# Kernel tuning notes

Hardware: AMD Instinct MI355X
Metric: run time of the kernel (lower is better)

Reference implementation:

```python
import jax, jax.numpy as jnp
import numpy as np

N, D_IN, D_HID, D_OUT, ORDER = 8192, 512, 1024, 64, 3

def setup_inputs() -> dict:
    key = jax.random.key(0)
    k = jax.random.split(key, 5)
    x = jax.random.normal(k[0], (N, D_IN), dtype=jnp.float32)
    adj = jax.random.uniform(k[1], (ORDER, N, N), dtype=jnp.float32)
    W1 = jax.random.normal(k[2], (ORDER, D_IN, D_HID), dtype=jnp.float32) * (1.0 / np.sqrt(D_IN))
    b1 = jnp.zeros((D_HID,), dtype=jnp.float32)
    W2 = jax.random.normal(k[3], (ORDER, D_HID, D_OUT), dtype=jnp.float32) * (1.0 / np.sqrt(D_HID))
    b2 = jnp.zeros((D_OUT,), dtype=jnp.float32)
    return {"x": x, "preprocessed": adj, "W1": W1, "b1": b1, "W2": W2, "b2": b2}

def multi_val_gc(x, adj, W, b):
    # x: [N, in], adj: [order, N, N], W: [order, in, out]
    xw = jnp.einsum('ni,kio->kno', x, W)          # [order, N, out]
    out = jnp.einsum('knm,kmo->no', adj, xw)      # sum over orders
    return out + b

def reference(x, preprocessed, W1, b1, W2, b2):
    h = multi_val_gc(x, preprocessed, W1, b1)
    h = jax.nn.relu(h)
    # dropout is identity in eval mode
    h = multi_val_gc(h, preprocessed, W2, b2)
    return jax.nn.log_softmax(h, axis=1)
```

## Files before the change

kernel.cpp:

```cpp
#include <hip/hip_runtime.h>
#include <hip/hip_bf16.h>
#include <cstdint>
#include <cstddef>


typedef __bf16 bf16_t;
typedef __bf16 bf16x8 __attribute__((ext_vector_type(8)));
typedef __bf16 bf16x4 __attribute__((ext_vector_type(4)));
typedef float  f32x4  __attribute__((ext_vector_type(4)));

#define NROWS 8192
#define DIN   512
#define DHID  1024
#define DOUT  64
#define ORD   3
#define KTOT  24576

#define GLDS(g, l) __builtin_amdgcn_global_load_lds( \
    (__attribute__((address_space(1))) void*)(g),    \
    (__attribute__((address_space(3))) void*)(l), 16, 0, 0)


__global__ void k_cvt_x(const float* __restrict__ x, bf16_t* __restrict__ xb) {
  int i = blockIdx.x * blockDim.x + threadIdx.x;
  const float4* p = reinterpret_cast<const float4*>(x) + (size_t)i * 2;
  float4 v0 = p[0], v1 = p[1];
  bf16x8 o;
  o[0]=(bf16_t)v0.x; o[1]=(bf16_t)v0.y; o[2]=(bf16_t)v0.z; o[3]=(bf16_t)v0.w;
  o[4]=(bf16_t)v1.x; o[5]=(bf16_t)v1.y; o[6]=(bf16_t)v1.z; o[7]=(bf16_t)v1.w;
  *reinterpret_cast<bf16x8*>(xb + (size_t)i * 8) = o;
}

__global__ void k_cvt_adj(const float* __restrict__ a, bf16_t* __restrict__ ab) {
  size_t i = (size_t)blockIdx.x * blockDim.x + threadIdx.x;
  const size_t stride = (size_t)gridDim.x * blockDim.x;
  const float4* src = reinterpret_cast<const float4*>(a);
#pragma unroll 4
  for (int it = 0; it < 48; ++it, i += stride) {
    float4 v0 = src[i * 2], v1 = src[i * 2 + 1];
    bf16x8 o;
    o[0]=(bf16_t)v0.x; o[1]=(bf16_t)v0.y; o[2]=(bf16_t)v0.z; o[3]=(bf16_t)v0.w;
    o[4]=(bf16_t)v1.x; o[5]=(bf16_t)v1.y; o[6]=(bf16_t)v1.z; o[7]=(bf16_t)v1.w;
    *reinterpret_cast<bf16x8*>(ab + i * 8) = o;
  }
}

__global__ void k_transpose_cvt(const float* __restrict__ src, bf16_t* __restrict__ dst,
                                int R, int C) {
  __shared__ float tile[64][65];
  int ord = blockIdx.z;
  src += (size_t)ord * R * C;
  dst += (size_t)ord * R * C;
  int c0 = blockIdx.x * 64, r0 = blockIdx.y * 64;
  for (int i = 0; i < 16; ++i) {
    int idx = i * 256 + threadIdx.x;
    int r = idx >> 6, c = idx & 63;
    tile[r][c] = src[(size_t)(r0 + r) * C + c0 + c];
  }
  __syncthreads();
  for (int i = 0; i < 16; ++i) {
    int idx = i * 256 + threadIdx.x;
    int cc = idx >> 6, rr = idx & 63;
    dst[(size_t)(c0 + cc) * R + r0 + rr] = (bf16_t)tile[rr][cc];
  }
}

__global__ __launch_bounds__(256) void k_gemm_xw1(
    const bf16_t* __restrict__ xb,
    const bf16_t* __restrict__ w1t,
    bf16_t* __restrict__ xw1t)
{
  __shared__ bf16_t As[128 * 64];
  __shared__ bf16_t Bs[128 * 64];
  int ntile = blockIdx.x, mtile = blockIdx.y, ord = blockIdx.z;
  int tid = threadIdx.x, lane = tid & 63, wid = tid >> 6;
  int wm = wid >> 1, wn = wid & 1;
  int sl = (lane & 7) ^ (lane >> 3);
  f32x4 acc[4][4] = {};
  const bf16_t* w1o = w1t + (size_t)ord * DHID * DIN;
  for (int kt = 0; kt < DIN; kt += 64) {
    for (int j = 0; j < 4; ++j) {
      int q = wid * 4 + j;
      int row = q * 8 + (lane >> 3);
      GLDS(xb + (size_t)(mtile * 128 + row) * DIN + kt + sl * 8, &As[q * 512]);
    }
    for (int j = 0; j < 4; ++j) {
      int q = wid * 4 + j;
      int row = q * 8 + (lane >> 3);
      GLDS(w1o + (size_t)(ntile * 128 + row) * DIN + kt + sl * 8, &Bs[q * 512]);
    }
    __syncthreads();
    for (int ks = 0; ks < 2; ++ks) {
      int psl = ((ks << 2) + (lane >> 4)) ^ (lane & 7);
      bf16x8 a[4], b[4];
      for (int f = 0; f < 4; ++f)
        a[f] = *reinterpret_cast<const bf16x8*>(&As[(wm * 64 + f * 16 + (lane & 15)) * 64 + psl * 8]);
      for (int f = 0; f < 4; ++f)
        b[f] = *reinterpret_cast<const bf16x8*>(&Bs[(wn * 64 + f * 16 + (lane & 15)) * 64 + psl * 8]);
      for (int fm = 0; fm < 4; ++fm)
        for (int fn = 0; fn < 4; ++fn)
          acc[fm][fn] = __builtin_amdgcn_mfma_f32_16x16x32_bf16(a[fm], b[fn], acc[fm][fn], 0, 0, 0);
    }
    __syncthreads();
  }
  for (int fm = 0; fm < 4; ++fm)
    for (int fn = 0; fn < 4; ++fn) {
      int o  = ntile * 128 + wn * 64 + fn * 16 + (lane & 15);
      int n0 = mtile * 128 + wm * 64 + fm * 16 + ((lane >> 4) << 2);
      bf16x4 v;
      v[0] = (bf16_t)acc[fm][fn][0]; v[1] = (bf16_t)acc[fm][fn][1];
      v[2] = (bf16_t)acc[fm][fn][2]; v[3] = (bf16_t)acc[fm][fn][3];
      *reinterpret_cast<bf16x4*>(&xw1t[(size_t)o * KTOT + ord * NROWS + n0]) = v;
    }
}

__global__ __launch_bounds__(512) void k_gemm_h256(
    const bf16_t* __restrict__ adjb,
    const bf16_t* __restrict__ xw1t,
    float* __restrict__ hpart)
{
  __shared__ bf16_t As[2][256 * 64];
  __shared__ bf16_t Bs[2][256 * 64];
  int d = blockIdx.x;
  int xcd = d & 7;
  int s = d >> 3;
  int ksp = xcd & 1;
  int mtile = (xcd >> 1) * 8 + (s >> 2);
  int ntile = s & 3;
  int tid = threadIdx.x, lane = tid & 63, wid = tid >> 6;
  int wm = wid >> 2, wn = wid & 3;
  int sl = (lane & 7) ^ (lane >> 3);
  const size_t NN = (size_t)NROWS * NROWS;
  f32x4 acc[8][4] = {};
  const int T0 = ksp * 192, NT = 192;

  auto stage = [&](int buf, int t) {
    int kk = (T0 + t) * 64;
    int ord = kk >> 13, mcol = kk & 8191;
    const bf16_t* ao = adjb + (size_t)ord * NN + (size_t)(mtile * 256) * NROWS + mcol;
#pragma unroll
    for (int j = 0; j < 4; ++j) {
      int q = wid * 4 + j;
      int row = q * 8 + (lane >> 3);
      GLDS(ao + (size_t)row * NROWS + sl * 8, &As[buf][q * 512]);
    }
#pragma unroll
    for (int j = 0; j < 4; ++j) {
      int q = wid * 4 + j;
      int row = q * 8 + (lane >> 3);
      GLDS(xw1t + (size_t)(ntile * 256 + row) * KTOT + kk + sl * 8, &Bs[buf][q * 512]);
    }
  };

  auto compute = [&](int cur) {
    const bf16_t* Ac = &As[cur][0];
    const bf16_t* Bc = &Bs[cur][0];
#pragma unroll
    for (int ks = 0; ks < 2; ++ks) {
      int psl = ((ks << 2) + (lane >> 4)) ^ (lane & 7);
      bf16x8 a[8], b[4];
#pragma unroll
      for (int f = 0; f < 8; ++f)
        a[f] = *reinterpret_cast<const bf16x8*>(&Ac[(wm * 128 + f * 16 + (lane & 15)) * 64 + psl * 8]);
#pragma unroll
      for (int f = 0; f < 4; ++f)
        b[f] = *reinterpret_cast<const bf16x8*>(&Bc[(wn * 64 + f * 16 + (lane & 15)) * 64 + psl * 8]);
#pragma unroll
      for (int fm = 0; fm < 8; ++fm)
#pragma unroll
        for (int fn = 0; fn < 4; ++fn)
          acc[fm][fn] = __builtin_amdgcn_mfma_f32_16x16x32_bf16(a[fm], b[fn], acc[fm][fn], 0, 0, 0);
    }
  };

  stage(0, 0);
  for (int t = 0; t < NT - 1; ++t) {
    int cur = t & 1;
    stage(cur ^ 1, t + 1);
    asm volatile("s_waitcnt vmcnt(8)" ::: "memory");
    __builtin_amdgcn_s_barrier();
    compute(cur);
    asm volatile("" ::: "memory");
    __builtin_amdgcn_s_barrier();
  }
  asm volatile("s_waitcnt vmcnt(0)" ::: "memory");
  __builtin_amdgcn_s_barrier();
  compute((NT - 1) & 1);

  float* pout = hpart + (size_t)ksp * NROWS * DHID;
#pragma unroll
  for (int fm = 0; fm < 8; ++fm)
#pragma unroll
    for (int fn = 0; fn < 4; ++fn) {
      int o  = ntile * 256 + wn * 64 + fn * 16 + (lane & 15);
      int n0 = mtile * 256 + wm * 128 + fm * 16 + ((lane >> 4) << 2);
      for (int j = 0; j < 4; ++j)
        pout[(size_t)(n0 + j) * DHID + o] = acc[fm][fn][j];
    }
}

__global__ void k_reduce_h(const float* __restrict__ hpart, const float* __restrict__ b1,
                           bf16_t* __restrict__ h) {
  size_t i4 = (size_t)blockIdx.x * blockDim.x + threadIdx.x;
  size_t base = i4 * 4;
  int col = (int)(base & (DHID - 1));
  const size_t S = (size_t)NROWS * DHID;
  float4 p0 = *reinterpret_cast<const float4*>(hpart + base);
  float4 p1 = *reinterpret_cast<const float4*>(hpart + S + base);
  float4 bb = *reinterpret_cast<const float4*>(b1 + col);
  bf16x4 v;
  float t0 = p0.x + p1.x + bb.x; v[0] = (bf16_t)(t0 > 0.f ? t0 : 0.f);
  float t1 = p0.y + p1.y + bb.y; v[1] = (bf16_t)(t1 > 0.f ? t1 : 0.f);
  float t2 = p0.z + p1.z + bb.z; v[2] = (bf16_t)(t2 > 0.f ? t2 : 0.f);
  float t3 = p0.w + p1.w + bb.w; v[3] = (bf16_t)(t3 > 0.f ? t3 : 0.f);
  *reinterpret_cast<bf16x4*>(h + base) = v;
}

__global__ __launch_bounds__(256) void k_gemm_h128(
    const bf16_t* __restrict__ adjb, const bf16_t* __restrict__ xw1t,
    const float* __restrict__ b1, bf16_t* __restrict__ h)
{
  __shared__ bf16_t As[2][128 * 64];
  __shared__ bf16_t Bs[2][128 * 64];
  int d = blockIdx.x;
  int xcd = d & 7;
  int idx = d >> 3;
  int mtile = xcd * 8 + (idx >> 3);
  int ntile = idx & 7;
  int tid = threadIdx.x, lane = tid & 63, wid = tid >> 6;
  int wm = wid >> 1, wn = wid & 1;
  int sl = (lane & 7) ^ (lane >> 3);
  const size_t NN = (size_t)NROWS * NROWS;
  f32x4 acc[4][4] = {};
  const int NT = KTOT / 64;

  auto stage = [&](int buf, int kt) {
    int kk = kt * 64;
    int ord = kk >> 13, mcol = kk & 8191;
    const bf16_t* ao = adjb + (size_t)ord * NN + (size_t)(mtile * 128) * NROWS + mcol;
#pragma unroll
    for (int jj = 0; jj < 4; ++jj) {
      int q = wid * 4 + jj;
      int row = q * 8 + (lane >> 3);
      GLDS(ao + (size_t)row * NROWS + sl * 8, &As[buf][q * 512]);
    }
#pragma unroll
    for (int jj = 0; jj < 4; ++jj) {
      int q = wid * 4 + jj;
      int row = q * 8 + (lane >> 3);
      GLDS(xw1t + (size_t)(ntile * 128 + row) * KTOT + kk + sl * 8, &Bs[buf][q * 512]);
    }
  };
  auto compute = [&](int cur) {
    const bf16_t* Ac = &As[cur][0];
    const bf16_t* Bc = &Bs[cur][0];
#pragma unroll
    for (int ks = 0; ks < 2; ++ks) {
      int psl = ((ks << 2) + (lane >> 4)) ^ (lane & 7);
      bf16x8 a[4], b[4];
      for (int f = 0; f < 4; ++f)
        a[f] = *reinterpret_cast<const bf16x8*>(&Ac[(wm * 64 + f * 16 + (lane & 15)) * 64 + psl * 8]);
      for (int f = 0; f < 4; ++f)
        b[f] = *reinterpret_cast<const bf16x8*>(&Bc[(wn * 64 + f * 16 + (lane & 15)) * 64 + psl * 8]);
      for (int fm = 0; fm < 4; ++fm)
        for (int fn = 0; fn < 4; ++fn)
          acc[fm][fn] = __builtin_amdgcn_mfma_f32_16x16x32_bf16(a[fm], b[fn], acc[fm][fn], 0, 0, 0);
    }
  };

  stage(0, 0);
  for (int t = 0; t < NT - 1; ++t) {
    int cur = t & 1;
    stage(cur ^ 1, t + 1);
    asm volatile("s_waitcnt vmcnt(8)" ::: "memory");
    __builtin_amdgcn_s_barrier();
    compute(cur);
    asm volatile("" ::: "memory");
    __builtin_amdgcn_s_barrier();
  }
  asm volatile("s_waitcnt vmcnt(0)" ::: "memory");
  __builtin_amdgcn_s_barrier();
  compute((NT - 1) & 1);

  for (int fm = 0; fm < 4; ++fm)
    for (int fn = 0; fn < 4; ++fn) {
      int o  = ntile * 128 + wn * 64 + fn * 16 + (lane & 15);
      float bias = b1[o];
      int n0 = mtile * 128 + wm * 64 + fm * 16 + ((lane >> 4) << 2);
      for (int jj = 0; jj < 4; ++jj) {
        float v = acc[fm][fn][jj] + bias;
        v = v > 0.0f ? v : 0.0f;
        h[(size_t)(n0 + jj) * DHID + o] = (bf16_t)v;
      }
    }
}

__global__ __launch_bounds__(256) void k_gemm_xw2(
    const bf16_t* __restrict__ h,
    const bf16_t* __restrict__ w2t,
    bf16_t* __restrict__ xw2t)
{
  __shared__ bf16_t As[128 * 64];
  __shared__ bf16_t Bs[64 * 64];
  int mtile = blockIdx.x, ord = blockIdx.y;
  int tid = threadIdx.x, lane = tid & 63, wid = tid >> 6;
  int wm = wid >> 1, wn = wid & 1;
  int sl = (lane & 7) ^ (lane >> 3);
  f32x4 acc[4][2] = {};
  const bf16_t* w2o = w2t + (size_t)ord * DOUT * DHID;
  for (int kt = 0; kt < DHID; kt += 64) {
    for (int j = 0; j < 4; ++j) {
      int q = wid * 4 + j;
      int row = q * 8 + (lane >> 3);
      GLDS(h + (size_t)(mtile * 128 + row) * DHID + kt + sl * 8, &As[q * 512]);
    }
    for (int j = 0; j < 2; ++j) {
      int q = wid * 2 + j;
      int row = q * 8 + (lane >> 3);
      GLDS(w2o + (size_t)row * DHID + kt + sl * 8, &Bs[q * 512]);
    }
    __syncthreads();
    for (int ks = 0; ks < 2; ++ks) {
      int psl = ((ks << 2) + (lane >> 4)) ^ (lane & 7);
      bf16x8 a[4], b[2];
      for (int f = 0; f < 4; ++f)
        a[f] = *reinterpret_cast<const bf16x8*>(&As[(wm * 64 + f * 16 + (lane & 15)) * 64 + psl * 8]);
      for (int f = 0; f < 2; ++f)
        b[f] = *reinterpret_cast<const bf16x8*>(&Bs[(wn * 32 + f * 16 + (lane & 15)) * 64 + psl * 8]);
      for (int fm = 0; fm < 4; ++fm)
        for (int fn = 0; fn < 2; ++fn)
          acc[fm][fn] = __builtin_amdgcn_mfma_f32_16x16x32_bf16(a[fm], b[fn], acc[fm][fn], 0, 0, 0);
    }
    __syncthreads();
  }
  for (int fm = 0; fm < 4; ++fm)
    for (int fn = 0; fn < 2; ++fn) {
      int o2 = wn * 32 + fn * 16 + (lane & 15);
      int n0 = mtile * 128 + wm * 64 + fm * 16 + ((lane >> 4) << 2);
      bf16x4 v;
      v[0] = (bf16_t)acc[fm][fn][0]; v[1] = (bf16_t)acc[fm][fn][1];
      v[2] = (bf16_t)acc[fm][fn][2]; v[3] = (bf16_t)acc[fm][fn][3];
      *reinterpret_cast<bf16x4*>(&xw2t[(size_t)o2 * KTOT + ord * NROWS + n0]) = v;
    }
}

__global__ __launch_bounds__(256) void k_gemm_out(
    const bf16_t* __restrict__ adjb,
    const bf16_t* __restrict__ xw2t,
    float* __restrict__ part)
{
  __shared__ bf16_t As[128 * 64];
  __shared__ bf16_t Bs[64 * 64];
  int mtile = blockIdx.x, ksp = blockIdx.y;
  int tid = threadIdx.x, lane = tid & 63, wid = tid >> 6;
  int wm = wid >> 1, wn = wid & 1;
  int sl = (lane & 7) ^ (lane >> 3);
  const size_t NN = (size_t)NROWS * NROWS;
  f32x4 acc[4][2] = {};
  for (int kt = ksp * 24; kt < ksp * 24 + 24; ++kt) {
    int kk = kt * 64;
    int ord = kk >> 13, mcol = kk & 8191;
    const bf16_t* ao = adjb + (size_t)ord * NN + (size_t)(mtile * 128) * NROWS + mcol;
    for (int j = 0; j < 4; ++j) {
      int q = wid * 4 + j;
      int row = q * 8 + (lane >> 3);
      GLDS(ao + (size_t)row * NROWS + sl * 8, &As[q * 512]);
    }
    for (int j = 0; j < 2; ++j) {
      int q = wid * 2 + j;
      int row = q * 8 + (lane >> 3);
      GLDS(xw2t + (size_t)row * KTOT + kk + sl * 8, &Bs[q * 512]);
    }
    __syncthreads();
    for (int ks = 0; ks < 2; ++ks) {
      int psl = ((ks << 2) + (lane >> 4)) ^ (lane & 7);
      bf16x8 a[4], b[2];
      for (int f = 0; f < 4; ++f)
        a[f] = *reinterpret_cast<const bf16x8*>(&As[(wm * 64 + f * 16 + (lane & 15)) * 64 + psl * 8]);
      for (int f = 0; f < 2; ++f)
        b[f] = *reinterpret_cast<const bf16x8*>(&Bs[(wn * 32 + f * 16 + (lane & 15)) * 64 + psl * 8]);
      for (int fm = 0; fm < 4; ++fm)
        for (int fn = 0; fn < 2; ++fn)
          acc[fm][fn] = __builtin_amdgcn_mfma_f32_16x16x32_bf16(a[fm], b[fn], acc[fm][fn], 0, 0, 0);
    }
    __syncthreads();
  }
  float* pout = part + (size_t)ksp * NROWS * DOUT;
  for (int fm = 0; fm < 4; ++fm)
    for (int fn = 0; fn < 2; ++fn) {
      int o2 = wn * 32 + fn * 16 + (lane & 15);
      int n0 = mtile * 128 + wm * 64 + fm * 16 + ((lane >> 4) << 2);
      for (int j = 0; j < 4; ++j)
        pout[(size_t)(n0 + j) * DOUT + o2] = acc[fm][fn][j];
    }
}

__global__ void k_logsoftmax(const float* __restrict__ part, const float* __restrict__ b2,
                             float* __restrict__ out) {
  int wid = threadIdx.x >> 6, lane = threadIdx.x & 63;
  int n = blockIdx.x * 4 + wid;
  size_t s = (size_t)NROWS * DOUT;
  float v = b2[lane];
#pragma unroll
  for (int p = 0; p < 16; ++p)
    v += part[(size_t)p * s + (size_t)n * DOUT + lane];
  float mx = v;
  for (int d = 32; d; d >>= 1) mx = fmaxf(mx, __shfl_xor(mx, d));
  float e = expf(v - mx);
  float sum = e;
  for (int d = 32; d; d >>= 1) sum += __shfl_xor(sum, d);
  out[(size_t)n * DOUT + lane] = (v - mx) - logf(sum);
}

__global__ __launch_bounds__(256) void k_gemm_h_f32(
    const float* __restrict__ adj, const bf16_t* __restrict__ xw1t,
    const float* __restrict__ b1, bf16_t* __restrict__ h)
{
  __shared__ bf16_t As[128 * 64];
  __shared__ bf16_t Bs[128 * 64];
  int d = blockIdx.x;
  int xcd = d & 7, idx = d >> 3;
  int mtile = xcd * 8 + (idx >> 3), ntile = idx & 7;
  int tid = threadIdx.x, lane = tid & 63, wid = tid >> 6;
  int wm = wid >> 1, wn = wid & 1;
  int sl = (lane & 7) ^ (lane >> 3);
  f32x4 acc[4][4] = {};
  for (int kt = 0; kt < KTOT / 64; ++kt) {
    int kk0 = kt * 64;
    int ord = kk0 >> 13, mcol = kk0 & 8191;
    for (int j = 0; j < 4; ++j) {
      int q = wid * 4 + j;
      int row = q * 8 + (lane >> 3);
      GLDS(xw1t + (size_t)(ntile * 128 + row) * KTOT + kk0 + sl * 8, &Bs[q * 512]);
    }
    const float* abase = adj + (size_t)ord * NROWS * NROWS + (size_t)(mtile * 128) * NROWS + mcol;
    bf16x8 st[4]; int mrow[4], kb[4];
    for (int i = 0; i < 4; ++i) {
      int c = i * 256 + tid;
      mrow[i] = c >> 3; kb[i] = c & 7;
      const float4* p = reinterpret_cast<const float4*>(abase + (size_t)mrow[i] * NROWS + kb[i] * 8);
      float4 v0 = p[0], v1 = p[1];
      bf16x8 o;
      o[0]=(bf16_t)v0.x; o[1]=(bf16_t)v0.y; o[2]=(bf16_t)v0.z; o[3]=(bf16_t)v0.w;
      o[4]=(bf16_t)v1.x; o[5]=(bf16_t)v1.y; o[6]=(bf16_t)v1.z; o[7]=(bf16_t)v1.w;
      st[i] = o;
    }
    for (int i = 0; i < 4; ++i)
      *reinterpret_cast<bf16x8*>(&As[mrow[i] * 64 + (kb[i] ^ (mrow[i] & 7)) * 8]) = st[i];
    __syncthreads();
    for (int ks = 0; ks < 2; ++ks) {
      int psl = ((ks << 2) + (lane >> 4)) ^ (lane & 7);
      bf16x8 a[4], b[4];
      for (int f = 0; f < 4; ++f)
        a[f] = *reinterpret_cast<const bf16x8*>(&As[(wm * 64 + f * 16 + (lane & 15)) * 64 + psl * 8]);
      for (int f = 0; f < 4; ++f)
        b[f] = *reinterpret_cast<const bf16x8*>(&Bs[(wn * 64 + f * 16 + (lane & 15)) * 64 + psl * 8]);
      for (int fm = 0; fm < 4; ++fm)
        for (int fn = 0; fn < 4; ++fn)
          acc[fm][fn] = __builtin_amdgcn_mfma_f32_16x16x32_bf16(a[fm], b[fn], acc[fm][fn], 0, 0, 0);
    }
    __syncthreads();
  }
  for (int fm = 0; fm < 4; ++fm)
    for (int fn = 0; fn < 4; ++fn) {
      int o  = ntile * 128 + wn * 64 + fn * 16 + (lane & 15);
      float bias = b1[o];
      int n0 = mtile * 128 + wm * 64 + fm * 16 + ((lane >> 4) << 2);
      for (int j = 0; j < 4; ++j) {
        float v = acc[fm][fn][j] + bias;
        v = v > 0.0f ? v : 0.0f;
        h[(size_t)(n0 + j) * DHID + o] = (bf16_t)v;
      }
    }
}

__global__ __launch_bounds__(256) void k_gemm_out_f32(
    const float* __restrict__ adj, const bf16_t* __restrict__ xw2t,
    float* __restrict__ part)
{
  __shared__ bf16_t As[128 * 64];
  __shared__ bf16_t Bs[64 * 64];
  int mtile = blockIdx.x, ksp = blockIdx.y;
  int tid = threadIdx.x, lane = tid & 63, wid = tid >> 6;
  int wm = wid >> 1, wn = wid & 1;
  int sl = (lane & 7) ^ (lane >> 3);
  f32x4 acc[4][2] = {};
  for (int kt = ksp * 24; kt < ksp * 24 + 24; ++kt) {
    int kk0 = kt * 64;
    int ord = kk0 >> 13, mcol = kk0 & 8191;
    for (int j = 0; j < 2; ++j) {
      int q = wid * 2 + j;
      int row = q * 8 + (lane >> 3);
      GLDS(xw2t + (size_t)row * KTOT + kk0 + sl * 8, &Bs[q * 512]);
    }
    const float* abase = adj + (size_t)ord * NROWS * NROWS + (size_t)(mtile * 128) * NROWS + mcol;
    bf16x8 st[4]; int mrow[4], kb[4];
    for (int i = 0; i < 4; ++i) {
      int c = i * 256 + tid;
      mrow[i] = c >> 3; kb[i] = c & 7;
      const float4* p = reinterpret_cast<const float4*>(abase + (size_t)mrow[i] * NROWS + kb[i] * 8);
      float4 v0 = p[0], v1 = p[1];
      bf16x8 o;
      o[0]=(bf16_t)v0.x; o[1]=(bf16_t)v0.y; o[2]=(bf16_t)v0.z; o[3]=(bf16_t)v0.w;
      o[4]=(bf16_t)v1.x; o[5]=(bf16_t)v1.y; o[6]=(bf16_t)v1.z; o[7]=(bf16_t)v1.w;
      st[i] = o;
    }
    for (int i = 0; i < 4; ++i)
      *reinterpret_cast<bf16x8*>(&As[mrow[i] * 64 + (kb[i] ^ (mrow[i] & 7)) * 8]) = st[i];
    __syncthreads();
    for (int ks = 0; ks < 2; ++ks) {
      int psl = ((ks << 2) + (lane >> 4)) ^ (lane & 7);
      bf16x8 a[4], b[2];
      for (int f = 0; f < 4; ++f)
        a[f] = *reinterpret_cast<const bf16x8*>(&As[(wm * 64 + f * 16 + (lane & 15)) * 64 + psl * 8]);
      for (int f = 0; f < 2; ++f)
        b[f] = *reinterpret_cast<const bf16x8*>(&Bs[(wn * 32 + f * 16 + (lane & 15)) * 64 + psl * 8]);
      for (int fm = 0; fm < 4; ++fm)
        for (int fn = 0; fn < 2; ++fn)
          acc[fm][fn] = __builtin_amdgcn_mfma_f32_16x16x32_bf16(a[fm], b[fn], acc[fm][fn], 0, 0, 0);
    }
    __syncthreads();
  }
  float* pout = part + (size_t)ksp * NROWS * DOUT;
  for (int fm = 0; fm < 4; ++fm)
    for (int fn = 0; fn < 2; ++fn) {
      int o2 = wn * 32 + fn * 16 + (lane & 15);
      int n0 = mtile * 128 + wm * 64 + fm * 16 + ((lane >> 4) << 2);
      for (int j = 0; j < 4; ++j)
        pout[(size_t)(n0 + j) * DOUT + o2] = acc[fm][fn][j];
    }
}

extern "C" void kernel_launch(void* const* d_in, const int* in_sizes, int n_in,
                              void* d_out, int out_size, void* d_ws, size_t ws_size,
                              hipStream_t stream) {
  const float* x   = (const float*)d_in[0];
  const float* adj = (const float*)d_in[1];
  const float* W1  = (const float*)d_in[2];
  const float* b1  = (const float*)d_in[3];
  const float* W2  = (const float*)d_in[4];
  const float* b2  = (const float*)d_in[5];
  float* out = (float*)d_out;
  char* ws = (char*)d_ws;

  const size_t ADJB_SZ  = 402653184ULL;
  const size_t NEED_OLD = 484835328ULL;
  const size_t NEED_NEW = 551944192ULL;

  if (ws_size >= NEED_OLD) {
    bf16_t* adjb = (bf16_t*)(ws + 0);
    bf16_t* xb   = (bf16_t*)(ws + ADJB_SZ);
    bf16_t* w1t  = (bf16_t*)(ws + ADJB_SZ + 8388608);
    bf16_t* w2t  = (bf16_t*)(ws + ADJB_SZ + 11534336);
    bf16_t* xw1t = (bf16_t*)(ws + ADJB_SZ + 11927552);
    bf16_t* h    = (bf16_t*)(ws + ADJB_SZ + 62259200);
    bf16_t* xw2t = (bf16_t*)(ws + ADJB_SZ + 79036416);
    float*  hpart = (float*)(ws + ADJB_SZ + 82182144);
    float*  part = (ws_size >= NEED_NEW) ? hpart
                                         : (float*)(ws + ADJB_SZ + 11927552);

    k_cvt_adj<<<2048, 256, 0, stream>>>(adj, adjb);
    k_cvt_x<<<2048, 256, 0, stream>>>(x, xb);
    k_transpose_cvt<<<dim3(16, 8, 3), 256, 0, stream>>>(W1, w1t, DIN, DHID);
    k_transpose_cvt<<<dim3(1, 16, 3), 256, 0, stream>>>(W2, w2t, DHID, DOUT);
    k_gemm_xw1<<<dim3(8, 64, 3), 256, 0, stream>>>(xb, w1t, xw1t);
    if (ws_size >= NEED_NEW) {
      k_gemm_h256<<<256, 512, 0, stream>>>(adjb, xw1t, hpart);
      k_reduce_h<<<8192, 256, 0, stream>>>(hpart, b1, h);
    } else {
      k_gemm_h128<<<512, 256, 0, stream>>>(adjb, xw1t, b1, h);
    }
    k_gemm_xw2<<<dim3(64, 3), 256, 0, stream>>>(h, w2t, xw2t);
    k_gemm_out<<<dim3(64, 16), 256, 0, stream>>>(adjb, xw2t, part);
    k_logsoftmax<<<2048, 256, 0, stream>>>(part, b2, out);
  } else {
    bf16_t* xb   = (bf16_t*)(ws + 0);
    bf16_t* w1t  = (bf16_t*)(ws + 8388608);
    bf16_t* w2t  = (bf16_t*)(ws + 11534336);
    bf16_t* xw1t = (bf16_t*)(ws + 11927552);
    bf16_t* h    = (bf16_t*)(ws + 62259200);
    bf16_t* xw2t = (bf16_t*)(ws + 79036416);
    float*  part = (float*)(ws + 11927552);

    k_cvt_x<<<2048, 256, 0, stream>>>(x, xb);
    k_transpose_cvt<<<dim3(16, 8, 3), 256, 0, stream>>>(W1, w1t, DIN, DHID);
    k_transpose_cvt<<<dim3(1, 16, 3), 256, 0, stream>>>(W2, w2t, DHID, DOUT);
    k_gemm_xw1<<<dim3(8, 64, 3), 256, 0, stream>>>(xb, w1t, xw1t);
    k_gemm_h_f32<<<512, 256, 0, stream>>>(adj, xw1t, b1, h);
    k_gemm_xw2<<<dim3(64, 3), 256, 0, stream>>>(h, w2t, xw2t);
    k_gemm_out_f32<<<dim3(64, 16), 256, 0, stream>>>(adj, xw2t, part);
    k_logsoftmax<<<2048, 256, 0, stream>>>(part, b2, out);
  }
}
```

Baseline: 889.4 us.

## Interleave LDS fragment loads with MFMA in ping-pong phases using setprio

Restructures the main GEMM loop so B fragments for both k-steps are loaded once per tile, then A fragments are loaded in four small phases, each followed by a block of MFMAs. Workgroup barriers, sched_barriers and s_setprio bracket every MFMA phase so waves alternate between LDS loads and matrix math, in the style of a ping-pong schedule. The goal is to overlap LDS reads with MFMA issue and lower register pressure. In exchange it adds many extra barriers per tile, which can stall waves if the phases are unbalanced.

```diff
diff --git a/kernel.cpp b/kernel.cpp
--- a/kernel.cpp
+++ b/kernel.cpp
@@ -152,40 +152,57 @@
     }
   };
 
-  auto compute = [&](int cur) {
+  stage(0, 0);
+  for (int t = 0; t < NT; ++t) {
+    int cur = t & 1;
+    if (t + 1 < NT) {
+      stage(cur ^ 1, t + 1);
+      asm volatile("s_waitcnt vmcnt(8)" ::: "memory");
+    } else {
+      asm volatile("s_waitcnt vmcnt(0)" ::: "memory");
+    }
+    __builtin_amdgcn_s_barrier();
+    __builtin_amdgcn_sched_barrier(0);
+
     const bf16_t* Ac = &As[cur][0];
     const bf16_t* Bc = &Bs[cur][0];
+    bf16x8 b[4][2];
 #pragma unroll
     for (int ks = 0; ks < 2; ++ks) {
       int psl = ((ks << 2) + (lane >> 4)) ^ (lane & 7);
-      bf16x8 a[8], b[4];
-#pragma unroll
-      for (int f = 0; f < 8; ++f)
-        a[f] = *reinterpret_cast<const bf16x8*>(&Ac[(wm * 128 + f * 16 + (lane & 15)) * 64 + psl * 8]);
-#pragma unroll
-      for (int f = 0; f < 4; ++f)
-        b[f] = *reinterpret_cast<const bf16x8*>(&Bc[(wn * 64 + f * 16 + (lane & 15)) * 64 + psl * 8]);
-#pragma unroll
-      for (int fm = 0; fm < 8; ++fm)
+#pragma unroll
+      for (int f = 0; f < 4; ++f)
+        b[f][ks] = *reinterpret_cast<const bf16x8*>(&Bc[(wn * 64 + f * 16 + (lane & 15)) * 64 + psl * 8]);
+    }
+#pragma unroll
+    for (int p = 0; p < 4; ++p) {
+      bf16x8 a[2][2];
+#pragma unroll
+      for (int ks = 0; ks < 2; ++ks) {
+        int psl = ((ks << 2) + (lane >> 4)) ^ (lane & 7);
+#pragma unroll
+        for (int f = 0; f < 2; ++f)
+          a[f][ks] = *reinterpret_cast<const bf16x8*>(
+              &Ac[(wm * 128 + (2 * p + f) * 16 + (lane & 15)) * 64 + psl * 8]);
+      }
+      __builtin_amdgcn_sched_barrier(0);
+      __builtin_amdgcn_s_barrier();
+      __builtin_amdgcn_sched_barrier(0);
+      __builtin_amdgcn_s_setprio(1);
+#pragma unroll
+      for (int f = 0; f < 2; ++f)
 #pragma unroll
         for (int fn = 0; fn < 4; ++fn)
-          acc[fm][fn] = __builtin_amdgcn_mfma_f32_16x16x32_bf16(a[fm], b[fn], acc[fm][fn], 0, 0, 0);
-    }
-  };
-
-  stage(0, 0);
-  for (int t = 0; t < NT - 1; ++t) {
-    int cur = t & 1;
-    stage(cur ^ 1, t + 1);
-    asm volatile("s_waitcnt vmcnt(8)" ::: "memory");
-    __builtin_amdgcn_s_barrier();
-    compute(cur);
-    asm volatile("" ::: "memory");
-    __builtin_amdgcn_s_barrier();
-  }
-  asm volatile("s_waitcnt vmcnt(0)" ::: "memory");
-  __builtin_amdgcn_s_barrier();
-  compute((NT - 1) & 1);
+#pragma unroll
+          for (int ks = 0; ks < 2; ++ks)
+            acc[2 * p + f][fn] = __builtin_amdgcn_mfma_f32_16x16x32_bf16(
+                a[f][ks], b[fn][ks], acc[2 * p + f][fn], 0, 0, 0);
+      __builtin_amdgcn_s_setprio(0);
+      __builtin_amdgcn_sched_barrier(0);
+      __builtin_amdgcn_s_barrier();
+      __builtin_amdgcn_sched_barrier(0);
+    }
+  }
 
   float* pout = hpart + (size_t)ksp * NROWS * DHID;
 #pragma unroll
```

Result: slower. 965.4 us (+8.6%).

## Load B fragments directly from global into registers, dropping B LDS staging

Applied to the files above, without the earlier changes.

Removes the shared-memory buffer for the xw1t operand in the big adjacency GEMM and has each wave load its B fragments straight from global memory into registers. The compute loop is also restructured to load A fragments per row-tile and interleave the two k-steps. This halves LDS footprint and LDS write/read traffic, but B loads are no longer shared across waves, are not prefetched, and their latency sits right before the barrier wait.

```diff
diff --git a/kernel.cpp b/kernel.cpp
--- a/kernel.cpp
+++ b/kernel.cpp
@@ -120,7 +120,6 @@
     float* __restrict__ hpart)
 {
   __shared__ bf16_t As[2][256 * 64];
-  __shared__ bf16_t Bs[2][256 * 64];
   int d = blockIdx.x;
   int xcd = d & 7;
   int s = d >> 3;
@@ -134,6 +133,9 @@
   f32x4 acc[8][4] = {};
   const int T0 = ksp * 192, NT = 192;
 
+  const bf16_t* bbase = xw1t
+      + (size_t)(ntile * 256 + wn * 64 + (lane & 15)) * KTOT + (lane >> 4) * 8;
+
   auto stage = [&](int buf, int t) {
     int kk = (T0 + t) * 64;
     int ord = kk >> 13, mcol = kk & 8191;
@@ -144,48 +146,44 @@
       int row = q * 8 + (lane >> 3);
       GLDS(ao + (size_t)row * NROWS + sl * 8, &As[buf][q * 512]);
     }
-#pragma unroll
-    for (int j = 0; j < 4; ++j) {
-      int q = wid * 4 + j;
-      int row = q * 8 + (lane >> 3);
-      GLDS(xw1t + (size_t)(ntile * 256 + row) * KTOT + kk + sl * 8, &Bs[buf][q * 512]);
-    }
   };
 
-  auto compute = [&](int cur) {
+  stage(0, 0);
+  for (int t = 0; t < NT; ++t) {
+    int cur = t & 1;
+    int kk = (T0 + t) * 64;
+    bf16x8 b[4][2];
+#pragma unroll
+    for (int fn = 0; fn < 4; ++fn)
+#pragma unroll
+      for (int ks = 0; ks < 2; ++ks)
+        b[fn][ks] = *reinterpret_cast<const bf16x8*>(
+            bbase + (size_t)(fn * 16) * KTOT + kk + ks * 32);
+    asm volatile("" ::: "memory");
+    if (t + 1 < NT) {
+      stage(cur ^ 1, t + 1);
+      asm volatile("s_waitcnt vmcnt(4)" ::: "memory");
+    } else {
+      asm volatile("s_waitcnt vmcnt(0)" ::: "memory");
+    }
+    __builtin_amdgcn_s_barrier();
     const bf16_t* Ac = &As[cur][0];
-    const bf16_t* Bc = &Bs[cur][0];
-#pragma unroll
-    for (int ks = 0; ks < 2; ++ks) {
-      int psl = ((ks << 2) + (lane >> 4)) ^ (lane & 7);
-      bf16x8 a[8], b[4];
-#pragma unroll
-      for (int f = 0; f < 8; ++f)
-        a[f] = *reinterpret_cast<const bf16x8*>(&Ac[(wm * 128 + f * 16 + (lane & 15)) * 64 + psl * 8]);
-#pragma unroll
-      for (int f = 0; f < 4; ++f)
-        b[f] = *reinterpret_cast<const bf16x8*>(&Bc[(wn * 64 + f * 16 + (lane & 15)) * 64 + psl * 8]);
-#pragma unroll
-      for (int fm = 0; fm < 8; ++fm)
-#pragma unroll
-        for (int fn = 0; fn < 4; ++fn)
-          acc[fm][fn] = __builtin_amdgcn_mfma_f32_16x16x32_bf16(a[fm], b[fn], acc[fm][fn], 0, 0, 0);
-    }
-  };
-
-  stage(0, 0);
-  for (int t = 0; t < NT - 1; ++t) {
-    int cur = t & 1;
-    stage(cur ^ 1, t + 1);
-    asm volatile("s_waitcnt vmcnt(8)" ::: "memory");
-    __builtin_amdgcn_s_barrier();
-    compute(cur);
+#pragma unroll
+    for (int fm = 0; fm < 8; ++fm) {
+      int rbase = (wm * 128 + fm * 16 + (lane & 15)) * 64;
+      int p0 = ((lane >> 4)) ^ (lane & 7);
+      int p1 = (4 + (lane >> 4)) ^ (lane & 7);
+      bf16x8 a0 = *reinterpret_cast<const bf16x8*>(&Ac[rbase + p0 * 8]);
+      bf16x8 a1 = *reinterpret_cast<const bf16x8*>(&Ac[rbase + p1 * 8]);
+#pragma unroll
+      for (int fn = 0; fn < 4; ++fn) {
+        acc[fm][fn] = __builtin_amdgcn_mfma_f32_16x16x32_bf16(a0, b[fn][0], acc[fm][fn], 0, 0, 0);
+        acc[fm][fn] = __builtin_amdgcn_mfma_f32_16x16x32_bf16(a1, b[fn][1], acc[fm][fn], 0, 0, 0);
+      }
+    }
     asm volatile("" ::: "memory");
     __builtin_amdgcn_s_barrier();
   }
-  asm volatile("s_waitcnt vmcnt(0)" ::: "memory");
-  __builtin_amdgcn_s_barrier();
-  compute((NT - 1) & 1);
 
   float* pout = hpart + (size_t)ksp * NROWS * DHID;
 #pragma unroll
```

Measured after the change: 1.070 ms. 1.2x slower.
